# Performance work log

Measured on AMD Instinct MI355X. Metric: run time of the kernel, lower is better.

The kernel has to match this reference:

```python
import jax, jax.numpy as jnp
import numpy as np

B, T, I, H, O = 64, 512, 256, 512, 256

def setup_inputs() -> dict:
    key = jax.random.key(0)
    ks = jax.random.split(key, 12)
    s = 1.0 / np.sqrt(H)
    u = lambda k, shp: jax.random.uniform(k, shp, jnp.float32, -s, s)
    return {
        'x': jax.random.normal(ks[0], (B, T, I), jnp.float32),
        'w_ih0': u(ks[1], (H, I)),  'w_hh0': u(ks[2], (H, H)),
        'b_ih0': u(ks[3], (H,)),    'b_hh0': u(ks[4], (H,)),
        'w_ih1': u(ks[5], (H, H)),  'w_hh1': u(ks[6], (H, H)),
        'b_ih1': u(ks[7], (H,)),    'b_hh1': u(ks[8], (H,)),
        'fc_w': u(ks[9], (O, H)),   'fc_b': u(ks[10], (O,)),
    }

def _rnn_layer(inp, w_ih, w_hh, b_ih, b_hh):
    # inp: [B, T, F] -> precompute input projection once (one big GEMM)
    xp = jnp.einsum('btf,hf->bth', inp, w_ih) + b_ih + b_hh  # [B, T, H]
    def step(h, xt):
        h = jnp.tanh(xt + h @ w_hh.T)  # [B, H]
        return h, h
    h0 = jnp.zeros((inp.shape[0], w_hh.shape[0]), inp.dtype)
    hT, outs = jax.lax.scan(step, h0, jnp.swapaxes(xp, 0, 1))  # outs: [T, B, H]
    return jnp.swapaxes(outs, 0, 1), hT

def reference(x, w_ih0, w_hh0, b_ih0, b_hh0, w_ih1, w_hh1, b_ih1, b_hh1, fc_w, fc_b):
    out0, h0f = _rnn_layer(x, w_ih0, w_hh0, b_ih0, b_hh0)
    out1, h1f = _rnn_layer(out0, w_ih1, w_hh1, b_ih1, b_hh1)
    hidden = jnp.stack([h0f, h1f])                  # [n_layers, B, H]
    out = out1.reshape(-1, out1.shape[-1]) @ fc_w.T + fc_b  # [B*T, O]
    return out, hidden
```

## Files before the change

kernel.cpp:

```cpp
#include <hip/hip_runtime.h>

#define B_  64
#define T_  512
#define I_  256
#define H_  512
#define O_  256
#define SENT 0x7F7F7F7Fu

typedef __attribute__((ext_vector_type(8))) __bf16 bf16x8;
typedef __attribute__((ext_vector_type(4))) float f32x4;
typedef unsigned int u32x4 __attribute__((ext_vector_type(4)));

__device__ __forceinline__ unsigned short f2bf(float f) {
    unsigned int u = __float_as_uint(f);
    unsigned int r = (u + 0x7fffu + ((u >> 16) & 1u)) >> 16;
    return (unsigned short)r;
}

__device__ __forceinline__ float tanh_fast(float x) {
    float e = __expf(2.0f * x);
    float d = e + 1.0f;
    float r;
    asm("v_rcp_f32 %0, %1" : "=v"(r) : "v"(d));
    return 1.0f - 2.0f * r;
}

__global__ void cvt_kernel(const float* __restrict__ in, unsigned short* __restrict__ out, int n4) {
    int i = blockIdx.x * blockDim.x + threadIdx.x;
    if (i >= n4) return;
    float4 f = reinterpret_cast<const float4*>(in)[i];
    ushort4 o;
    o.x = f2bf(f.x); o.y = f2bf(f.y); o.z = f2bf(f.z); o.w = f2bf(f.w);
    reinterpret_cast<ushort4*>(out)[i] = o;
}

__global__ __launch_bounds__(256) void gemm_kernel(
    const unsigned short* __restrict__ A,
    const unsigned short* __restrict__ Bw,
    const float* __restrict__ b0,
    const float* __restrict__ b1,
    float* __restrict__ C,
    int M, int N, int K, int perm, int histA)
{
    const int m0 = blockIdx.x * 64;
    const int n0 = blockIdx.y * 64;
    const int tid = threadIdx.x;
    const int wv = tid >> 6;
    const int l = tid & 63;
    const int lr = l & 15;
    const int lk = (l >> 4) * 8;
    const int arow = m0 + wv * 16 + lr;

    size_t abase;
    if (histA) {
        int b = arow >> 9, t = arow & 511;
        int g = b >> 4, r = b & 15;
        abase = ((size_t)(g * 512 + t) * 16 + r) * 512;
    } else {
        abase = (size_t)arow * K;
    }

    f32x4 acc[4] = {{0,0,0,0},{0,0,0,0},{0,0,0,0},{0,0,0,0}};
    const int nks = K / 32;
    for (int ks = 0; ks < nks; ++ks) {
        bf16x8 a = *reinterpret_cast<const bf16x8*>(A + abase + ks * 32 + lk);
        #pragma unroll
        for (int nt = 0; nt < 4; ++nt) {
            bf16x8 b = *reinterpret_cast<const bf16x8*>(Bw + (size_t)(n0 + nt * 16 + lr) * K + ks * 32 + lk);
            acc[nt] = __builtin_amdgcn_mfma_f32_16x16x32_bf16(a, b, acc[nt], 0, 0, 0);
        }
    }
    #pragma unroll
    for (int nt = 0; nt < 4; ++nt) {
        #pragma unroll
        for (int r = 0; r < 4; ++r) {
            int row = m0 + wv * 16 + (l >> 4) * 4 + r;
            int col = n0 + nt * 16 + lr;
            float v = acc[nt][r];
            if (b0) v += b0[col];
            if (b1) v += b1[col];
            int cs = perm ? ((col & 15) * 32 + (col >> 4)) : col;
            C[(size_t)row * N + cs] = v;
        }
    }
}

#define LDW8(ARR, BASE) \
    asm volatile( \
        "global_load_dwordx4 %0, %8, %9 offset:0\n\t" \
        "global_load_dwordx4 %1, %8, %9 offset:64\n\t" \
        "global_load_dwordx4 %2, %8, %9 offset:128\n\t" \
        "global_load_dwordx4 %3, %8, %9 offset:192\n\t" \
        "global_load_dwordx4 %4, %8, %9 offset:256\n\t" \
        "global_load_dwordx4 %5, %8, %9 offset:320\n\t" \
        "global_load_dwordx4 %6, %8, %9 offset:384\n\t" \
        "global_load_dwordx4 %7, %8, %9 offset:448\n\t" \
        "s_waitcnt vmcnt(0)" \
        : "=&v"(ARR[0]), "=&v"(ARR[1]), "=&v"(ARR[2]), "=&v"(ARR[3]), \
          "=&v"(ARR[4]), "=&v"(ARR[5]), "=&v"(ARR[6]), "=&v"(ARR[7]) \
        : "v"(BASE), "s"(w))

#define LOAD_XP_PEER(XPQ, AFP, VSLR) \
    asm volatile( \
        "global_load_dwordx4 %0, %12, %16\n\t" \
        "global_load_dwordx4 %1, %13, %16\n\t" \
        "global_load_dwordx4 %2, %14, %16\n\t" \
        "global_load_dwordx4 %3, %15, %16\n\t" \
        "global_load_dwordx4 %4, %17, %18 sc0 sc1\n\t" \
        "global_load_dwordx4 %5, %17, %18 offset:64 sc0 sc1\n\t" \
        "global_load_dwordx4 %6, %17, %18 offset:128 sc0 sc1\n\t" \
        "global_load_dwordx4 %7, %17, %18 offset:192 sc0 sc1\n\t" \
        "global_load_dwordx4 %8, %17, %18 offset:256 sc0 sc1\n\t" \
        "global_load_dwordx4 %9, %17, %18 offset:320 sc0 sc1\n\t" \
        "global_load_dwordx4 %10, %17, %18 offset:384 sc0 sc1\n\t" \
        "global_load_dwordx4 %11, %17, %18 offset:448 sc0 sc1\n\t" \
        "s_waitcnt vmcnt(0)" \
        : "=&v"(XPQ[0]), "=&v"(XPQ[1]), "=&v"(XPQ[2]), "=&v"(XPQ[3]), \
          "=&v"(AFP[0]), "=&v"(AFP[1]), "=&v"(AFP[2]), "=&v"(AFP[3]), \
          "=&v"(AFP[4]), "=&v"(AFP[5]), "=&v"(AFP[6]), "=&v"(AFP[7]) \
        : "v"(vxpr[0]), "v"(vxpr[1]), "v"(vxpr[2]), "v"(vxpr[3]), \
          "s"(xpg), "v"(VSLR), "s"(histg))

#define RETRY8(AFP, VSLR) \
    asm volatile( \
        "global_load_dwordx4 %0, %8, %9 sc0 sc1\n\t" \
        "global_load_dwordx4 %1, %8, %9 offset:64 sc0 sc1\n\t" \
        "global_load_dwordx4 %2, %8, %9 offset:128 sc0 sc1\n\t" \
        "global_load_dwordx4 %3, %8, %9 offset:192 sc0 sc1\n\t" \
        "global_load_dwordx4 %4, %8, %9 offset:256 sc0 sc1\n\t" \
        "global_load_dwordx4 %5, %8, %9 offset:320 sc0 sc1\n\t" \
        "global_load_dwordx4 %6, %8, %9 offset:384 sc0 sc1\n\t" \
        "global_load_dwordx4 %7, %8, %9 offset:448 sc0 sc1\n\t" \
        "s_waitcnt vmcnt(0)" \
        : "=&v"(AFP[0]), "=&v"(AFP[1]), "=&v"(AFP[2]), "=&v"(AFP[3]), \
          "=&v"(AFP[4]), "=&v"(AFP[5]), "=&v"(AFP[6]), "=&v"(AFP[7]) \
        : "v"(VSLR), "s"(histg))

#define SENT_CHECK(AFP, BAD) \
    { BAD = 0; \
      _Pragma("unroll") \
      for (int _i = 0; _i < 8; ++_i) \
          _Pragma("unroll") \
          for (int _j = 0; _j < 4; ++_j) \
              BAD |= (AFP[_i][_j] == SENT); }

#define STORE16(PK, VHW) \
    asm volatile( \
        "global_store_dword %16, %0, %17 sc0 sc1\n\t" \
        "global_store_dword %16, %1, %17 offset:1024 sc0 sc1\n\t" \
        "global_store_dword %16, %2, %17 offset:2048 sc0 sc1\n\t" \
        "global_store_dword %16, %3, %17 offset:3072 sc0 sc1\n\t" \
        "global_store_dword %16, %4, %17 offset:32 sc0 sc1\n\t" \
        "global_store_dword %16, %5, %17 offset:1056 sc0 sc1\n\t" \
        "global_store_dword %16, %6, %17 offset:2080 sc0 sc1\n\t" \
        "global_store_dword %16, %7, %17 offset:3104 sc0 sc1\n\t" \
        "global_store_dword %16, %8, %17 offset:64 sc0 sc1\n\t" \
        "global_store_dword %16, %9, %17 offset:1088 sc0 sc1\n\t" \
        "global_store_dword %16, %10, %17 offset:2112 sc0 sc1\n\t" \
        "global_store_dword %16, %11, %17 offset:3136 sc0 sc1\n\t" \
        "global_store_dword %16, %12, %17 offset:96 sc0 sc1\n\t" \
        "global_store_dword %16, %13, %17 offset:1120 sc0 sc1\n\t" \
        "global_store_dword %16, %14, %17 offset:2144 sc0 sc1\n\t" \
        "global_store_dword %16, %15, %17 offset:3168 sc0 sc1" \
        :: "v"(PK[0]), "v"(PK[1]), "v"(PK[2]), "v"(PK[3]), \
           "v"(PK[4]), "v"(PK[5]), "v"(PK[6]), "v"(PK[7]), \
           "v"(PK[8]), "v"(PK[9]), "v"(PK[10]), "v"(PK[11]), \
           "v"(PK[12]), "v"(PK[13]), "v"(PK[14]), "v"(PK[15]), \
           "v"(VHW), "s"(histg) \
        : "memory")

__global__ __launch_bounds__(256, 1) void recur_kernel(
    const float* __restrict__ xp,
    const unsigned short* __restrict__ w,
    unsigned short* __restrict__ hist,
    float* __restrict__ h_final)
{
    __shared__ __align__(16) unsigned short lds[16 * 280];

    const int bid = blockIdx.x;
    const int g   = bid >> 1;
    const int jw  = bid & 1;
    const int pjw = jw ^ 1;
    const int b0  = g * 16;
    const int tid = threadIdx.x;
    const int wv  = tid >> 6;
    const int l   = tid & 63;
    const int lr  = l & 15;
    const int lk  = (l >> 4) * 8;
    const int jn0 = jw * 256 + wv * 64;
    const int erow_l = (l >> 4) * 4;

    const float*    xpg   = xp + (size_t)b0 * T_ * H_;
    unsigned short* histg = hist + (size_t)g * T_ * 16 * 512;
    float*          hfg   = h_final + (size_t)b0 * H_;

    bf16x8 bwo[4][8], bwp[4][8];
    #pragma unroll
    for (int nt = 0; nt < 4; ++nt) {
        unsigned int vo = (unsigned)((jn0 + nt * 16 + lr) * (H_ * 2) + jw  * 512 + lk * 2);
        unsigned int vp = (unsigned)((jn0 + nt * 16 + lr) * (H_ * 2) + pjw * 512 + lk * 2);
        LDW8(bwo[nt], vo);
        LDW8(bwp[nt], vp);
    }

    unsigned int vxpr[4];
    #pragma unroll
    for (int r = 0; r < 4; ++r)
        vxpr[r] = (unsigned)(((erow_l + r) * T_ * H_ + lr * 32 + jw * 16 + wv * 4) * 4);
    const unsigned int vslr0 = (unsigned)(lr * 1024 + pjw * 512 + lk * 2);
    const unsigned int vhw0  = (unsigned)(erow_l * 1024 + (jn0 + lr) * 2);
    const int cb = wv * 32 + (lr >> 1);

    {
        f32x4 xpq[4];
        asm volatile(
            "global_load_dwordx4 %0, %4, %8\n\t"
            "global_load_dwordx4 %1, %5, %8\n\t"
            "global_load_dwordx4 %2, %6, %8\n\t"
            "global_load_dwordx4 %3, %7, %8\n\t"
            "s_waitcnt vmcnt(0)"
            : "=&v"(xpq[0]), "=&v"(xpq[1]), "=&v"(xpq[2]), "=&v"(xpq[3])
            : "v"(vxpr[0]), "v"(vxpr[1]), "v"(vxpr[2]), "v"(vxpr[3]), "s"(xpg));
        unsigned int pk[16];
        #pragma unroll
        for (int nt = 0; nt < 4; ++nt)
            #pragma unroll
            for (int r = 0; r < 4; ++r) {
                float hv = tanh_fast(xpq[r][nt]);
                unsigned int mine = f2bf(hv);
                unsigned int oth = (unsigned int)__shfl_xor((int)mine, 1, 64);
                pk[nt * 4 + r] = mine | (oth << 16);
            }
        if (!(lr & 1)) {
            unsigned int* lw = (unsigned int*)lds;
            #pragma unroll
            for (int nt = 0; nt < 4; ++nt)
                #pragma unroll
                for (int r = 0; r < 4; ++r)
                    lw[(erow_l + r) * 140 + cb + nt * 8] = pk[nt * 4 + r];
            STORE16(pk, vhw0);
        }
        __syncthreads();
        #pragma unroll
        for (int r = 0; r < 4; ++r) vxpr[r] += H_ * 4;
    }

    for (int t = 1; t < T_; ++t) {
        f32x4 acc[4] = {{0,0,0,0},{0,0,0,0},{0,0,0,0},{0,0,0,0}};
        {
            bf16x8 afo[8];
            const unsigned short* lrb = lds + lr * 280 + lk;
            #pragma unroll
            for (int i = 0; i < 8; ++i)
                afo[i] = *reinterpret_cast<const bf16x8*>(lrb + i * 32);
            #pragma unroll
            for (int i = 0; i < 8; ++i) {
                acc[0] = __builtin_amdgcn_mfma_f32_16x16x32_bf16(afo[i], bwo[0][i], acc[0], 0, 0, 0);
                acc[1] = __builtin_amdgcn_mfma_f32_16x16x32_bf16(afo[i], bwo[1][i], acc[1], 0, 0, 0);
                acc[2] = __builtin_amdgcn_mfma_f32_16x16x32_bf16(afo[i], bwo[2][i], acc[2], 0, 0, 0);
                acc[3] = __builtin_amdgcn_mfma_f32_16x16x32_bf16(afo[i], bwo[3][i], acc[3], 0, 0, 0);
            }
        }
        __syncthreads();

        const unsigned int vslr = vslr0 + (unsigned)(t - 1) * 16384u;
        f32x4 xpq[4];
        u32x4 afp[8];
        LOAD_XP_PEER(xpq, afp, vslr);
        int bad;
        SENT_CHECK(afp, bad);
        while (__any(bad)) { RETRY8(afp, vslr); SENT_CHECK(afp, bad); }
        __builtin_amdgcn_sched_barrier(0);

        #pragma unroll
        for (int i = 0; i < 8; ++i) {
            bf16x8 a = __builtin_bit_cast(bf16x8, afp[i]);
            acc[0] = __builtin_amdgcn_mfma_f32_16x16x32_bf16(a, bwp[0][i], acc[0], 0, 0, 0);
            acc[1] = __builtin_amdgcn_mfma_f32_16x16x32_bf16(a, bwp[1][i], acc[1], 0, 0, 0);
            acc[2] = __builtin_amdgcn_mfma_f32_16x16x32_bf16(a, bwp[2][i], acc[2], 0, 0, 0);
            acc[3] = __builtin_amdgcn_mfma_f32_16x16x32_bf16(a, bwp[3][i], acc[3], 0, 0, 0);
        }

        unsigned int pk[16];
        #pragma unroll
        for (int nt = 0; nt < 4; ++nt)
            #pragma unroll
            for (int r = 0; r < 4; ++r) {
                float pre = acc[nt][r] + xpq[r][nt];
                float hv = tanh_fast(pre);
                if (t == T_ - 1)
                    hfg[(size_t)(erow_l + r) * H_ + jn0 + nt * 16 + lr] = hv;
                unsigned int mine = f2bf(hv);
                unsigned int oth = (unsigned int)__shfl_xor((int)mine, 1, 64);
                pk[nt * 4 + r] = mine | (oth << 16);
            }
        if (!(lr & 1)) {
            unsigned int* lw = (unsigned int*)lds;
            #pragma unroll
            for (int nt = 0; nt < 4; ++nt)
                #pragma unroll
                for (int r = 0; r < 4; ++r)
                    lw[(erow_l + r) * 140 + cb + nt * 8] = pk[nt * 4 + r];
            unsigned int vhw = vhw0 + (unsigned)t * 16384u;
            STORE16(pk, vhw);
        }

        __syncthreads();
        #pragma unroll
        for (int r = 0; r < 4; ++r) vxpr[r] += H_ * 4;
    }
}

#define OFF_XBF    ((size_t)0)
#define OFF_WIH0   ((size_t)16777216)
#define OFF_WHH0   ((size_t)17039360)
#define OFF_WIH1   ((size_t)17563648)
#define OFF_WHH1   ((size_t)18087936)
#define OFF_FCW    ((size_t)18612224)
#define OFF_XP     ((size_t)18874368)
#define OFF_HIST   ((size_t)85983232)
#define WS_NEED    ((size_t)119799808)

extern "C" void kernel_launch(void* const* d_in, const int* in_sizes, int n_in,
                              void* d_out, int out_size, void* d_ws, size_t ws_size,
                              hipStream_t stream) {
    if (ws_size < WS_NEED) return;
    const float* x     = (const float*)d_in[0];
    const float* w_ih0 = (const float*)d_in[1];
    const float* w_hh0 = (const float*)d_in[2];
    const float* b_ih0 = (const float*)d_in[3];
    const float* b_hh0 = (const float*)d_in[4];
    const float* w_ih1 = (const float*)d_in[5];
    const float* w_hh1 = (const float*)d_in[6];
    const float* b_ih1 = (const float*)d_in[7];
    const float* b_hh1 = (const float*)d_in[8];
    const float* fc_w  = (const float*)d_in[9];
    const float* fc_b  = (const float*)d_in[10];

    char* ws = (char*)d_ws;
    unsigned short* x_bf     = (unsigned short*)(ws + OFF_XBF);
    unsigned short* w_ih0_bf = (unsigned short*)(ws + OFF_WIH0);
    unsigned short* w_hh0_bf = (unsigned short*)(ws + OFF_WHH0);
    unsigned short* w_ih1_bf = (unsigned short*)(ws + OFF_WIH1);
    unsigned short* w_hh1_bf = (unsigned short*)(ws + OFF_WHH1);
    unsigned short* fc_w_bf  = (unsigned short*)(ws + OFF_FCW);
    float*          xp       = (float*)(ws + OFF_XP);
    unsigned short* hist     = (unsigned short*)(ws + OFF_HIST);

    float* out  = (float*)d_out;
    float* hid0 = out + (size_t)B_ * T_ * O_;
    float* hid1 = hid0 + (size_t)B_ * H_;

    auto cvt = [&](const float* in, unsigned short* o, int n) {
        int n4 = n / 4;
        cvt_kernel<<<(n4 + 255) / 256, 256, 0, stream>>>(in, o, n4);
    };
    cvt(x,     x_bf,     B_ * T_ * I_);
    cvt(w_ih0, w_ih0_bf, H_ * I_);
    cvt(w_hh0, w_hh0_bf, H_ * H_);
    cvt(w_ih1, w_ih1_bf, H_ * H_);
    cvt(w_hh1, w_hh1_bf, H_ * H_);
    cvt(fc_w,  fc_w_bf,  O_ * H_);

    const int M = B_ * T_;

    gemm_kernel<<<dim3(M / 64, H_ / 64), 256, 0, stream>>>(
        x_bf, w_ih0_bf, b_ih0, b_hh0, xp, M, H_, I_, 1, 0);

    hipMemsetAsync(ws + OFF_HIST, 0x7F, 33554432, stream);
    recur_kernel<<<8, 256, 0, stream>>>(xp, w_hh0_bf, hist, hid0);

    gemm_kernel<<<dim3(M / 64, H_ / 64), 256, 0, stream>>>(
        hist, w_ih1_bf, b_ih1, b_hh1, xp, M, H_, H_, 1, 1);

    hipMemsetAsync(ws + OFF_HIST, 0x7F, 33554432, stream);
    recur_kernel<<<8, 256, 0, stream>>>(xp, w_hh1_bf, hist, hid1);

    gemm_kernel<<<dim3(M / 64, O_ / 64), 256, 0, stream>>>(
        hist, fc_w_bf, fc_b, nullptr, out, M, O_, H_, 0, 1);
}
```

Measured before the change: 4.243 ms.

## Exchange hidden state via small ring-buffer slots instead of full history

The recurrent kernel now swaps half-hidden-states between paired blocks through a 4-slot ring buffer in workspace. Each slot is reset to the sentinel after use, so the 32MB memset of the full history per layer is no longer needed. Outputs go to a plain row-major bf16 buffer with deferred, non-coherent stores, which simplifies GEMM addressing. The next step's xp loads are issued early to overlap with the sync, and polling alternates cache-scope modes. Launching 16 blocks with half returning early spreads the active blocks across dies differently. This risks slot-reuse races, since correctness depends on the 4-deep ring and the sentinel resets.

Measured after the change: 4.307 ms. No clear change (+1.5%).

```diff
diff --git a/kernel.cpp b/kernel.cpp
--- a/kernel.cpp
+++ b/kernel.cpp
@@ -6,6 +6,7 @@
 #define H_  512
 #define O_  256
 #define SENT 0x7F7F7F7Fu
+#define SLOT_BYTES 8192u
 
 typedef __attribute__((ext_vector_type(8))) __bf16 bf16x8;
 typedef __attribute__((ext_vector_type(4))) float f32x4;
@@ -40,7 +41,7 @@
     const float* __restrict__ b0,
     const float* __restrict__ b1,
     float* __restrict__ C,
-    int M, int N, int K, int perm, int histA)
+    int M, int N, int K, int perm)
 {
     const int m0 = blockIdx.x * 64;
     const int n0 = blockIdx.y * 64;
@@ -51,19 +52,10 @@
     const int lk = (l >> 4) * 8;
     const int arow = m0 + wv * 16 + lr;
 
-    size_t abase;
-    if (histA) {
-        int b = arow >> 9, t = arow & 511;
-        int g = b >> 4, r = b & 15;
-        abase = ((size_t)(g * 512 + t) * 16 + r) * 512;
-    } else {
-        abase = (size_t)arow * K;
-    }
-
     f32x4 acc[4] = {{0,0,0,0},{0,0,0,0},{0,0,0,0},{0,0,0,0}};
     const int nks = K / 32;
     for (int ks = 0; ks < nks; ++ks) {
-        bf16x8 a = *reinterpret_cast<const bf16x8*>(A + abase + ks * 32 + lk);
+        bf16x8 a = *reinterpret_cast<const bf16x8*>(A + (size_t)arow * K + ks * 32 + lk);
         #pragma unroll
         for (int nt = 0; nt < 4; ++nt) {
             bf16x8 b = *reinterpret_cast<const bf16x8*>(Bw + (size_t)(n0 + nt * 16 + lr) * K + ks * 32 + lk);
@@ -100,41 +92,39 @@
           "=&v"(ARR[4]), "=&v"(ARR[5]), "=&v"(ARR[6]), "=&v"(ARR[7]) \
         : "v"(BASE), "s"(w))
 
-#define LOAD_XP_PEER(XPQ, AFP, VSLR) \
-    asm volatile( \
-        "global_load_dwordx4 %0, %12, %16\n\t" \
-        "global_load_dwordx4 %1, %13, %16\n\t" \
-        "global_load_dwordx4 %2, %14, %16\n\t" \
-        "global_load_dwordx4 %3, %15, %16\n\t" \
-        "global_load_dwordx4 %4, %17, %18 sc0 sc1\n\t" \
-        "global_load_dwordx4 %5, %17, %18 offset:64 sc0 sc1\n\t" \
-        "global_load_dwordx4 %6, %17, %18 offset:128 sc0 sc1\n\t" \
-        "global_load_dwordx4 %7, %17, %18 offset:192 sc0 sc1\n\t" \
-        "global_load_dwordx4 %8, %17, %18 offset:256 sc0 sc1\n\t" \
-        "global_load_dwordx4 %9, %17, %18 offset:320 sc0 sc1\n\t" \
-        "global_load_dwordx4 %10, %17, %18 offset:384 sc0 sc1\n\t" \
-        "global_load_dwordx4 %11, %17, %18 offset:448 sc0 sc1\n\t" \
+#define LOAD_XP4(XPQ) \
+    asm volatile( \
+        "global_load_dwordx4 %0, %4, %8\n\t" \
+        "global_load_dwordx4 %1, %5, %8\n\t" \
+        "global_load_dwordx4 %2, %6, %8\n\t" \
+        "global_load_dwordx4 %3, %7, %8\n\t" \
         "s_waitcnt vmcnt(0)" \
-        : "=&v"(XPQ[0]), "=&v"(XPQ[1]), "=&v"(XPQ[2]), "=&v"(XPQ[3]), \
-          "=&v"(AFP[0]), "=&v"(AFP[1]), "=&v"(AFP[2]), "=&v"(AFP[3]), \
-          "=&v"(AFP[4]), "=&v"(AFP[5]), "=&v"(AFP[6]), "=&v"(AFP[7]) \
-        : "v"(vxpr[0]), "v"(vxpr[1]), "v"(vxpr[2]), "v"(vxpr[3]), \
-          "s"(xpg), "v"(VSLR), "s"(histg))
-
-#define RETRY8(AFP, VSLR) \
-    asm volatile( \
-        "global_load_dwordx4 %0, %8, %9 sc0 sc1\n\t" \
-        "global_load_dwordx4 %1, %8, %9 offset:64 sc0 sc1\n\t" \
-        "global_load_dwordx4 %2, %8, %9 offset:128 sc0 sc1\n\t" \
-        "global_load_dwordx4 %3, %8, %9 offset:192 sc0 sc1\n\t" \
-        "global_load_dwordx4 %4, %8, %9 offset:256 sc0 sc1\n\t" \
-        "global_load_dwordx4 %5, %8, %9 offset:320 sc0 sc1\n\t" \
-        "global_load_dwordx4 %6, %8, %9 offset:384 sc0 sc1\n\t" \
-        "global_load_dwordx4 %7, %8, %9 offset:448 sc0 sc1\n\t" \
+        : "=&v"(XPQ[0]), "=&v"(XPQ[1]), "=&v"(XPQ[2]), "=&v"(XPQ[3]) \
+        : "v"(vxpr[0]), "v"(vxpr[1]), "v"(vxpr[2]), "v"(vxpr[3]), "s"(xpg))
+
+#define ISSUE_XP4(XPQ) \
+    asm volatile( \
+        "global_load_dwordx4 %0, %4, %8\n\t" \
+        "global_load_dwordx4 %1, %5, %8\n\t" \
+        "global_load_dwordx4 %2, %6, %8\n\t" \
+        "global_load_dwordx4 %3, %7, %8" \
+        : "=&v"(XPQ[0]), "=&v"(XPQ[1]), "=&v"(XPQ[2]), "=&v"(XPQ[3]) \
+        : "v"(vxpr[0]), "v"(vxpr[1]), "v"(vxpr[2]), "v"(vxpr[3]), "s"(xpg))
+
+#define POLL8(AFP, VSLR, SC) \
+    asm volatile( \
+        "global_load_dwordx4 %0, %8, %9 " SC "\n\t" \
+        "global_load_dwordx4 %1, %8, %9 offset:64 " SC "\n\t" \
+        "global_load_dwordx4 %2, %8, %9 offset:128 " SC "\n\t" \
+        "global_load_dwordx4 %3, %8, %9 offset:192 " SC "\n\t" \
+        "global_load_dwordx4 %4, %8, %9 offset:256 " SC "\n\t" \
+        "global_load_dwordx4 %5, %8, %9 offset:320 " SC "\n\t" \
+        "global_load_dwordx4 %6, %8, %9 offset:384 " SC "\n\t" \
+        "global_load_dwordx4 %7, %8, %9 offset:448 " SC "\n\t" \
         "s_waitcnt vmcnt(0)" \
         : "=&v"(AFP[0]), "=&v"(AFP[1]), "=&v"(AFP[2]), "=&v"(AFP[3]), \
           "=&v"(AFP[4]), "=&v"(AFP[5]), "=&v"(AFP[6]), "=&v"(AFP[7]) \
-        : "v"(VSLR), "s"(histg))
+        : "v"(VSLR), "s"(slR))
 
 #define SENT_CHECK(AFP, BAD) \
     { BAD = 0; \
@@ -144,42 +134,77 @@
           for (int _j = 0; _j < 4; ++_j) \
               BAD |= (AFP[_i][_j] == SENT); }
 
-#define STORE16(PK, VHW) \
+#define STORE_SLOT16(PK, VSLW) \
     asm volatile( \
         "global_store_dword %16, %0, %17 sc0 sc1\n\t" \
-        "global_store_dword %16, %1, %17 offset:1024 sc0 sc1\n\t" \
-        "global_store_dword %16, %2, %17 offset:2048 sc0 sc1\n\t" \
-        "global_store_dword %16, %3, %17 offset:3072 sc0 sc1\n\t" \
+        "global_store_dword %16, %1, %17 offset:512 sc0 sc1\n\t" \
+        "global_store_dword %16, %2, %17 offset:1024 sc0 sc1\n\t" \
+        "global_store_dword %16, %3, %17 offset:1536 sc0 sc1\n\t" \
         "global_store_dword %16, %4, %17 offset:32 sc0 sc1\n\t" \
-        "global_store_dword %16, %5, %17 offset:1056 sc0 sc1\n\t" \
-        "global_store_dword %16, %6, %17 offset:2080 sc0 sc1\n\t" \
-        "global_store_dword %16, %7, %17 offset:3104 sc0 sc1\n\t" \
+        "global_store_dword %16, %5, %17 offset:544 sc0 sc1\n\t" \
+        "global_store_dword %16, %6, %17 offset:1056 sc0 sc1\n\t" \
+        "global_store_dword %16, %7, %17 offset:1568 sc0 sc1\n\t" \
         "global_store_dword %16, %8, %17 offset:64 sc0 sc1\n\t" \
-        "global_store_dword %16, %9, %17 offset:1088 sc0 sc1\n\t" \
-        "global_store_dword %16, %10, %17 offset:2112 sc0 sc1\n\t" \
-        "global_store_dword %16, %11, %17 offset:3136 sc0 sc1\n\t" \
+        "global_store_dword %16, %9, %17 offset:576 sc0 sc1\n\t" \
+        "global_store_dword %16, %10, %17 offset:1088 sc0 sc1\n\t" \
+        "global_store_dword %16, %11, %17 offset:1600 sc0 sc1\n\t" \
         "global_store_dword %16, %12, %17 offset:96 sc0 sc1\n\t" \
-        "global_store_dword %16, %13, %17 offset:1120 sc0 sc1\n\t" \
-        "global_store_dword %16, %14, %17 offset:2144 sc0 sc1\n\t" \
-        "global_store_dword %16, %15, %17 offset:3168 sc0 sc1" \
+        "global_store_dword %16, %13, %17 offset:608 sc0 sc1\n\t" \
+        "global_store_dword %16, %14, %17 offset:1120 sc0 sc1\n\t" \
+        "global_store_dword %16, %15, %17 offset:1632 sc0 sc1" \
         :: "v"(PK[0]), "v"(PK[1]), "v"(PK[2]), "v"(PK[3]), \
            "v"(PK[4]), "v"(PK[5]), "v"(PK[6]), "v"(PK[7]), \
            "v"(PK[8]), "v"(PK[9]), "v"(PK[10]), "v"(PK[11]), \
            "v"(PK[12]), "v"(PK[13]), "v"(PK[14]), "v"(PK[15]), \
-           "v"(VHW), "s"(histg) \
+           "v"(VSLW), "s"(slW) \
         : "memory")
+
+#define OUT16(PK) \
+    asm volatile( \
+        "global_store_dword %16, %0, %20\n\t" \
+        "global_store_dword %17, %1, %20\n\t" \
+        "global_store_dword %18, %2, %20\n\t" \
+        "global_store_dword %19, %3, %20\n\t" \
+        "global_store_dword %16, %4, %20 offset:32\n\t" \
+        "global_store_dword %17, %5, %20 offset:32\n\t" \
+        "global_store_dword %18, %6, %20 offset:32\n\t" \
+        "global_store_dword %19, %7, %20 offset:32\n\t" \
+        "global_store_dword %16, %8, %20 offset:64\n\t" \
+        "global_store_dword %17, %9, %20 offset:64\n\t" \
+        "global_store_dword %18, %10, %20 offset:64\n\t" \
+        "global_store_dword %19, %11, %20 offset:64\n\t" \
+        "global_store_dword %16, %12, %20 offset:96\n\t" \
+        "global_store_dword %17, %13, %20 offset:96\n\t" \
+        "global_store_dword %18, %14, %20 offset:96\n\t" \
+        "global_store_dword %19, %15, %20 offset:96" \
+        :: "v"(PK[0]), "v"(PK[1]), "v"(PK[2]), "v"(PK[3]), \
+           "v"(PK[4]), "v"(PK[5]), "v"(PK[6]), "v"(PK[7]), \
+           "v"(PK[8]), "v"(PK[9]), "v"(PK[10]), "v"(PK[11]), \
+           "v"(PK[12]), "v"(PK[13]), "v"(PK[14]), "v"(PK[15]), \
+           "v"(vout[0]), "v"(vout[1]), "v"(vout[2]), "v"(vout[3]), \
+           "s"(out_bf) \
+        : "memory")
+
+#define SENTRESET(VS) \
+    asm volatile( \
+        "global_store_dwordx4 %0, %1, %2 sc0 sc1\n\t" \
+        "global_store_dwordx4 %0, %1, %2 offset:1024 sc0 sc1" \
+        :: "v"(VS), "v"(sentq), "s"(slR) : "memory")
 
 __global__ __launch_bounds__(256, 1) void recur_kernel(
     const float* __restrict__ xp,
     const unsigned short* __restrict__ w,
-    unsigned short* __restrict__ hist,
-    float* __restrict__ h_final)
+    unsigned short* __restrict__ out_bf,
+    float* __restrict__ h_final,
+    unsigned short* __restrict__ slots)
 {
     __shared__ __align__(16) unsigned short lds[16 * 280];
 
-    const int bid = blockIdx.x;
-    const int g   = bid >> 1;
-    const int jw  = bid & 1;
+    const int bid16 = blockIdx.x;
+    if (bid16 & 4) return;
+    const int g   = bid16 & 3;
+    const int jw  = (bid16 >> 3) & 1;
+    const int widx = g * 2 + jw;
     const int pjw = jw ^ 1;
     const int b0  = g * 16;
     const int tid = threadIdx.x;
@@ -189,10 +214,12 @@
     const int lk  = (l >> 4) * 8;
     const int jn0 = jw * 256 + wv * 64;
     const int erow_l = (l >> 4) * 4;
-
-    const float*    xpg   = xp + (size_t)b0 * T_ * H_;
-    unsigned short* histg = hist + (size_t)g * T_ * 16 * 512;
-    float*          hfg   = h_final + (size_t)b0 * H_;
+    const int erow_g = b0 + erow_l;
+
+    const float*          xpg = xp + (size_t)b0 * T_ * H_;
+    float*                hfg = h_final + (size_t)b0 * H_;
+    unsigned short*       slW = slots + (size_t)widx * 16384;
+    const unsigned short* slR = slots + (size_t)(widx ^ 1) * 16384;
 
     bf16x8 bwo[4][8], bwp[4][8];
     #pragma unroll
@@ -203,25 +230,23 @@
         LDW8(bwp[nt], vp);
     }
 
-    unsigned int vxpr[4];
+    unsigned int vxpr[4], vout[4];
     #pragma unroll
-    for (int r = 0; r < 4; ++r)
+    for (int r = 0; r < 4; ++r) {
         vxpr[r] = (unsigned)(((erow_l + r) * T_ * H_ + lr * 32 + jw * 16 + wv * 4) * 4);
-    const unsigned int vslr0 = (unsigned)(lr * 1024 + pjw * 512 + lk * 2);
-    const unsigned int vhw0  = (unsigned)(erow_l * 1024 + (jn0 + lr) * 2);
+        vout[r] = (unsigned)(((erow_g + r) * T_) * H_ * 2 + (jn0 + lr) * 2);
+    }
+    const unsigned int vslr0 = (unsigned)(lr * 512 + lk * 2);
+    const unsigned int vslw0 = (unsigned)(erow_l * 512 + (wv * 64 + lr) * 2);
+    const unsigned int vsent0 = (unsigned)(wv * 2048 + l * 16);
+    const u32x4 sentq = {SENT, SENT, SENT, SENT};
     const int cb = wv * 32 + (lr >> 1);
 
+    unsigned int pks[16];
+    f32x4 xpq[4];
+
     {
-        f32x4 xpq[4];
-        asm volatile(
-            "global_load_dwordx4 %0, %4, %8\n\t"
-            "global_load_dwordx4 %1, %5, %8\n\t"
-            "global_load_dwordx4 %2, %6, %8\n\t"
-            "global_load_dwordx4 %3, %7, %8\n\t"
-            "s_waitcnt vmcnt(0)"
-            : "=&v"(xpq[0]), "=&v"(xpq[1]), "=&v"(xpq[2]), "=&v"(xpq[3])
-            : "v"(vxpr[0]), "v"(vxpr[1]), "v"(vxpr[2]), "v"(vxpr[3]), "s"(xpg));
-        unsigned int pk[16];
+        LOAD_XP4(xpq);
         #pragma unroll
         for (int nt = 0; nt < 4; ++nt)
             #pragma unroll
@@ -229,7 +254,7 @@
                 float hv = tanh_fast(xpq[r][nt]);
                 unsigned int mine = f2bf(hv);
                 unsigned int oth = (unsigned int)__shfl_xor((int)mine, 1, 64);
-                pk[nt * 4 + r] = mine | (oth << 16);
+                pks[nt * 4 + r] = mine | (oth << 16);
             }
         if (!(lr & 1)) {
             unsigned int* lw = (unsigned int*)lds;
@@ -237,12 +262,14 @@
             for (int nt = 0; nt < 4; ++nt)
                 #pragma unroll
                 for (int r = 0; r < 4; ++r)
-                    lw[(erow_l + r) * 140 + cb + nt * 8] = pk[nt * 4 + r];
-            STORE16(pk, vhw0);
-        }
+                    lw[(erow_l + r) * 140 + cb + nt * 8] = pks[nt * 4 + r];
+            unsigned int vslw = vslw0 + 1u * SLOT_BYTES;
+            STORE_SLOT16(pks, vslw);
+        }
+        #pragma unroll
+        for (int r = 0; r < 4; ++r) vxpr[r] += H_ * 4;
+        ISSUE_XP4(xpq);
         __syncthreads();
-        #pragma unroll
-        for (int r = 0; r < 4; ++r) vxpr[r] += H_ * 4;
     }
 
     for (int t = 1; t < T_; ++t) {
@@ -263,14 +290,23 @@
         }
         __syncthreads();
 
-        const unsigned int vslr = vslr0 + (unsigned)(t - 1) * 16384u;
-        f32x4 xpq[4];
+        const unsigned int vslr = vslr0 + (unsigned)(t & 3) * SLOT_BYTES;
         u32x4 afp[8];
-        LOAD_XP_PEER(xpq, afp, vslr);
         int bad;
+        POLL8(afp, vslr, "sc0");
         SENT_CHECK(afp, bad);
-        while (__any(bad)) { RETRY8(afp, vslr); SENT_CHECK(afp, bad); }
+        while (__any(bad)) {
+            POLL8(afp, vslr, "sc0 sc1");
+            SENT_CHECK(afp, bad);
+            if (!__any(bad)) break;
+            POLL8(afp, vslr, "sc0");
+            SENT_CHECK(afp, bad);
+        }
         __builtin_amdgcn_sched_barrier(0);
+
+        if (!(lr & 1)) OUT16(pks);
+        #pragma unroll
+        for (int r = 0; r < 4; ++r) vout[r] += H_ * 2;
 
         #pragma unroll
         for (int i = 0; i < 8; ++i) {
@@ -281,7 +317,7 @@
             acc[3] = __builtin_amdgcn_mfma_f32_16x16x32_bf16(a, bwp[3][i], acc[3], 0, 0, 0);
         }
 
-        unsigned int pk[16];
+        unsigned int pkn[16];
         #pragma unroll
         for (int nt = 0; nt < 4; ++nt)
             #pragma unroll
@@ -292,7 +328,7 @@
                     hfg[(size_t)(erow_l + r) * H_ + jn0 + nt * 16 + lr] = hv;
                 unsigned int mine = f2bf(hv);
                 unsigned int oth = (unsigned int)__shfl_xor((int)mine, 1, 64);
-                pk[nt * 4 + r] = mine | (oth << 16);
+                pkn[nt * 4 + r] = mine | (oth << 16);
             }
         if (!(lr & 1)) {
             unsigned int* lw = (unsigned int*)lds;
@@ -300,15 +336,24 @@
             for (int nt = 0; nt < 4; ++nt)
                 #pragma unroll
                 for (int r = 0; r < 4; ++r)
-                    lw[(erow_l + r) * 140 + cb + nt * 8] = pk[nt * 4 + r];
-            unsigned int vhw = vhw0 + (unsigned)t * 16384u;
-            STORE16(pk, vhw);
-        }
+                    lw[(erow_l + r) * 140 + cb + nt * 8] = pkn[nt * 4 + r];
+            unsigned int vslw = vslw0 + (unsigned)((t + 1) & 3) * SLOT_BYTES;
+            STORE_SLOT16(pkn, vslw);
+        }
+        #pragma unroll
+        for (int r = 0; r < 4; ++r) vxpr[r] += H_ * 4;
+        if (t < T_ - 1) ISSUE_XP4(xpq);
+        #pragma unroll
+        for (int i = 0; i < 16; ++i) pks[i] = pkn[i];
 
         __syncthreads();
-        #pragma unroll
-        for (int r = 0; r < 4; ++r) vxpr[r] += H_ * 4;
-    }
+        {
+            unsigned int vs = vsent0 + (unsigned)(t & 3) * SLOT_BYTES;
+            SENTRESET(vs);
+        }
+    }
+
+    if (!(lr & 1)) OUT16(pks);
 }
 
 #define OFF_XBF    ((size_t)0)
@@ -318,7 +363,8 @@
 #define OFF_WHH1   ((size_t)18087936)
 #define OFF_FCW    ((size_t)18612224)
 #define OFF_XP     ((size_t)18874368)
-#define OFF_HIST   ((size_t)85983232)
+#define OFF_OUTBF  ((size_t)85983232)
+#define OFF_SLOTS  ((size_t)119537664)
 #define WS_NEED    ((size_t)119799808)
 
 extern "C" void kernel_launch(void* const* d_in, const int* in_sizes, int n_in,
@@ -345,11 +391,14 @@
     unsigned short* w_hh1_bf = (unsigned short*)(ws + OFF_WHH1);
     unsigned short* fc_w_bf  = (unsigned short*)(ws + OFF_FCW);
     float*          xp       = (float*)(ws + OFF_XP);
-    unsigned short* hist     = (unsigned short*)(ws + OFF_HIST);
+    unsigned short* out_bf   = (unsigned short*)(ws + OFF_OUTBF);
+    unsigned short* slots    = (unsigned short*)(ws + OFF_SLOTS);
 
     float* out  = (float*)d_out;
     float* hid0 = out + (size_t)B_ * T_ * O_;
     float* hid1 = hid0 + (size_t)B_ * H_;
+
+    hipMemsetAsync(ws + OFF_SLOTS, 0x7F, 262144, stream);
 
     auto cvt = [&](const float* in, unsigned short* o, int n) {
         int n4 = n / 4;
@@ -365,17 +414,17 @@
     const int M = B_ * T_;
 
     gemm_kernel<<<dim3(M / 64, H_ / 64), 256, 0, stream>>>(
-        x_bf, w_ih0_bf, b_ih0, b_hh0, xp, M, H_, I_, 1, 0);
-
-    hipMemsetAsync(ws + OFF_HIST, 0x7F, 33554432, stream);
-    recur_kernel<<<8, 256, 0, stream>>>(xp, w_hh0_bf, hist, hid0);
+        x_bf, w_ih0_bf, b_ih0, b_hh0, xp, M, H_, I_, 1);
+
+    recur_kernel<<<16, 256, 0, stream>>>(xp, w_hh0_bf, out_bf, hid0, slots);
 
     gemm_kernel<<<dim3(M / 64, H_ / 64), 256, 0, stream>>>(
-        hist, w_ih1_bf, b_ih1, b_hh1, xp, M, H_, H_, 1, 1);
-
-    hipMemsetAsync(ws + OFF_HIST, 0x7F, 33554432, stream);
-    recur_kernel<<<8, 256, 0, stream>>>(xp, w_hh1_bf, hist, hid1);
+        out_bf, w_ih1_bf, b_ih1, b_hh1, xp, M, H_, H_, 1);
+
+    hipMemsetAsync(ws + OFF_SLOTS, 0x7F, 262144, stream);
+
+    recur_kernel<<<16, 256, 0, stream>>>(xp, w_hh1_bf, out_bf, hid1, slots);
 
     gemm_kernel<<<dim3(M / 64, O_ / 64), 256, 0, stream>>>(
-        hist, fc_w_bf, fc_b, nullptr, out, M, O_, H_, 0, 1);
-}
+        out_bf, fc_w_bf, fc_b, nullptr, out, M, O_, H_, 0);
+}
```
